# Kernel tuning notes

Measured on AMD Instinct MI355X. Metric: run time of the kernel, lower is better.

## Reference

```python
import jax, jax.numpy as jnp
import numpy as np

BATCH, NUM_MASKS, IN_DIM, OUT_DIM = 512, 16, 1024, 1024


def setup_inputs() -> dict:
    key = jax.random.key(0)
    k1, k2, k3 = jax.random.split(key, 3)
    x = jax.random.normal(k1, (BATCH, NUM_MASKS, IN_DIM), dtype=jnp.float32)
    kernel = jax.random.normal(k2, (IN_DIM, OUT_DIM), dtype=jnp.float32) * (1.0 / np.sqrt(IN_DIM))
    masks = jax.random.uniform(k3, (NUM_MASKS, IN_DIM, OUT_DIM), dtype=jnp.float32)
    return {"x": x, "kernel": kernel, "masks": masks}


def reference(x, kernel, masks):
    # masked_kernel[m, i, o] = kernel[i, o] * masks[m, i, o]
    masked_kernel = kernel[None, :, :] * masks  # (M, I, O)
    # Original tf.scan serializes batch; equivalent math is one batched einsum:
    # out[b, m, o] = sum_i x[b, m, i] * masked_kernel[m, i, o]
    # NOTE: the executed tf.scan path applies NO activation, so neither do we.
    out = jnp.einsum('bmi,mio->bmo', x, masked_kernel)  # (B, M, O)
    return out
```

## Files before the change

### kernel.cpp

```cpp
#include <hip/hip_runtime.h>
#include <hip/hip_bf16.h>


#define BATCH 512
#define NMASK 16
#define IN_D  1024
#define OUT_D 1024

using bf16x8 = __attribute__((ext_vector_type(8))) __bf16;
using bf16x4 = __attribute__((ext_vector_type(4))) __bf16;
using f32x16 = __attribute__((ext_vector_type(16))) float;
using f32x4  = __attribute__((ext_vector_type(4))) float;
using f32x2  = __attribute__((ext_vector_type(2))) float;

typedef const __attribute__((address_space(1))) void gvoid_t;
typedef __attribute__((address_space(3))) void lvoid_t;

__device__ __forceinline__ void dma16(const void* g, const void* l) {
    __builtin_amdgcn_global_load_lds((gvoid_t*)(uintptr_t)g,
                                     (lvoid_t*)(uintptr_t)l, 16, 0, 0);
}

__global__ void __launch_bounds__(256, 8)
mdl_prep_w(const float* __restrict__ Kn,
           const float* __restrict__ Mk,
           unsigned short* __restrict__ Wt)
{
    const int raw = blockIdx.x;
    const int wg  = (raw & 7) * 1024 + (raw >> 3);
    const int m  = wg >> 9;
    const int G  = (wg >> 2) & 127;
    const int cq = wg & 3;
    const int col = cq * 256 + threadIdx.x;
    const int i0  = G * 8;

    const float* mk = Mk + ((size_t)m * IN_D + i0) * OUT_D + col;
    const float* kn = Kn + (size_t)i0 * OUT_D + col;

    float a[8], b[8];
#pragma unroll
    for (int r = 0; r < 8; ++r) {
        a[r] = mk[(size_t)r * OUT_D];
        b[r] = kn[(size_t)r * OUT_D];
    }
    bf16x8 g;
#pragma unroll
    for (int r = 0; r < 8; ++r)
        g[r] = (__bf16)(a[r] * b[r]);

    *(bf16x8*)(Wt + (((size_t)m * 128 + G) * 1024 + col) * 8) = g;
}

__global__ void __launch_bounds__(512, 4)
mdl_prep_x(const float* __restrict__ X,
           unsigned short* __restrict__ Xp)
{
    const int t  = threadIdx.x;
    const int b2 = blockIdx.x;
    const int strip = b2 >> 2;
    const int Gq    = b2 & 3;
    const int m  = strip >> 3;
    const int bt = strip & 7;
    const int row = t >> 3;
    const int oc  = t & 7;

    const float* src = X + ((size_t)(bt * 64 + row) * NMASK + m) * IN_D
                         + Gq * 256 + oc * 32;
    f32x4 av[8];
#pragma unroll
    for (int q = 0; q < 8; ++q)
        av[q] = *(const f32x4*)(src + q * 4);

    unsigned short* dstS = Xp + (size_t)strip * 65536
                              + (size_t)(Gq * 32 + oc * 4) * 512 + row * 8;
#pragma unroll
    for (int j = 0; j < 4; ++j) {
        bf16x8 g;
#pragma unroll
        for (int e = 0; e < 4; ++e) {
            g[e]     = (__bf16)av[2 * j][e];
            g[4 + e] = (__bf16)av[2 * j + 1][e];
        }
        *(bf16x8*)(dstS + (size_t)j * 512) = g;
    }
}

struct Frags { bf16x8 a[2][2]; bf16x8 b[2][2]; };

__global__ void __launch_bounds__(256, 2)
mdl_gemm2(const unsigned short* __restrict__ Xp,
          const unsigned short* __restrict__ Wt,
          float* __restrict__ Out)
{
    const int t = threadIdx.x;
    const int l = t & 63;
    const int w = t >> 6;

    const int raw = blockIdx.x;
    const int wg  = (raw & 7) * 64 + (raw >> 3);
    const int v   = wg * 4 + w;
    const int m   = v >> 7;
    const int v7  = v & 127;
    const int bt  = v7 >> 4;
    const int ot  = v7 & 15;

    const unsigned short* Ap = Xp + (size_t)(m * 8 + bt) * 65536;
    const int la = (l & 31) * 8;
    const int ls = l >> 5;
    const int bcol = ot * 64 + (l & 31);

    f32x16 acc[2][2];
#pragma unroll
    for (int ti = 0; ti < 2; ++ti)
#pragma unroll
        for (int tj = 0; tj < 2; ++tj)
#pragma unroll
            for (int e = 0; e < 16; ++e)
                acc[ti][tj][e] = 0.f;

    auto LOADF = [&](Frags& F, int kb) {
#pragma unroll
        for (int s = 0; s < 2; ++s) {
            const int G = (kb >> 3) + s * 2 + ls;
            const unsigned short* ab = Ap + (size_t)G * 512 + la;
            F.a[s][0] = *(const bf16x8*)(ab);
            F.a[s][1] = *(const bf16x8*)(ab + 256);
            const unsigned short* bb =
                Wt + (((size_t)m * 128 + G) * 1024 + bcol) * 8;
            F.b[s][0] = *(const bf16x8*)(bb);
            F.b[s][1] = *(const bf16x8*)(bb + 256);
        }
    };
    auto MF = [&](Frags& F) {
#pragma unroll
        for (int s = 0; s < 2; ++s)
#pragma unroll
            for (int ti = 0; ti < 2; ++ti)
#pragma unroll
                for (int tj = 0; tj < 2; ++tj)
                    acc[ti][tj] = __builtin_amdgcn_mfma_f32_32x32x16_bf16(
                        F.a[s][ti], F.b[s][tj], acc[ti][tj], 0, 0, 0);
    };

    Frags S0, S1;
    LOADF(S0, 0);
    for (int kb = 0; kb < IN_D; kb += 64) {
        LOADF(S1, kb + 32);
        __builtin_amdgcn_sched_barrier(0);
        MF(S0);
        LOADF(S0, (kb + 64) & (IN_D - 1));
        __builtin_amdgcn_sched_barrier(0);
        MF(S1);
    }

    const int r0 = bt * 64 + 4 * ls;
    const int c0 = ot * 64 + (l & 31);
#pragma unroll
    for (int ti = 0; ti < 2; ++ti) {
#pragma unroll
        for (int tj = 0; tj < 2; ++tj) {
#pragma unroll
            for (int g = 0; g < 4; ++g) {
#pragma unroll
                for (int q = 0; q < 4; ++q) {
                    const int row = r0 + ti * 32 + g * 8 + q;
                    const int col = c0 + tj * 32;
                    Out[((size_t)row * NMASK + m) * OUT_D + col] =
                        acc[ti][tj][g * 4 + q];
                }
            }
        }
    }
}

#define FAKP 40
#define FBKP 34
#define FMFSZ (32 * 128)

__global__ void __launch_bounds__(512, 4)
mdl_fused_fallback(const float* __restrict__ X,
                   const float* __restrict__ Kn,
                   const float* __restrict__ Mk,
                   float* __restrict__ Out)
{
    __shared__ __align__(16) float          Mf[3 * FMFSZ];
    __shared__ __align__(16) unsigned short As[128 * FAKP];
    __shared__ __align__(16) unsigned short Bs[128 * FBKP];

    const int t = threadIdx.x;
    const int l = t & 63;
    const int w = t >> 6;

    const int raw = blockIdx.x;
    const int wg  = (raw & 7) * 64 + (raw >> 3);
    const int m   = wg >> 5;
    const int ob  = (wg >> 2) & 7;
    const int bb  = wg & 3;

    const int wr = w >> 2, wc = w & 3;

    f32x4 acc[4][2];
#pragma unroll
    for (int mi = 0; mi < 4; ++mi)
#pragma unroll
        for (int ni = 0; ni < 2; ++ni)
            acc[mi][ni] = (f32x4){0.f, 0.f, 0.f, 0.f};

    const int a_row = t >> 2;
    const int a_kh  = (t & 3) * 8;
    const int o2 = (t & 63) * 2;
    const int k4 = w * 4;

    const int obase = ob * 128;
    const float* Xa  = X + ((size_t)(bb * 128 + a_row) * NMASK + m) * IN_D + a_kh;
    const float* Knb = Kn + obase + o2;
    const float* Mkm = Mk + (size_t)m * IN_D * OUT_D;

    auto DMA = [&](int tile, int c) {
        const int kt = tile * 32;
#pragma unroll
        for (int j = 0; j < 2; ++j) {
            const int k = j * 16 + w * 2 + (l >> 5);
            const float* gsrc = Mkm + (size_t)(kt + k) * OUT_D + obase + (l & 31) * 4;
            dma16(gsrc, &Mf[c * FMFSZ + j * 2048 + w * 256]);
        }
    };

    DMA(0, 0);
    DMA(1, 1);
    asm volatile("s_waitcnt vmcnt(2)" ::: "memory");
    __builtin_amdgcn_sched_barrier(0);
    __builtin_amdgcn_s_barrier();
    __builtin_amdgcn_sched_barrier(0);

    int c_cur = 0, c_nxt = 1, c_far = 2;

    for (int tt = 0; tt < 32; ++tt) {
        const int kt = tt * 32;
        f32x4 xv0 = *(const f32x4*)(Xa + kt);
        f32x4 xv1 = *(const f32x4*)(Xa + kt + 4);
        f32x2 kv[4];
#pragma unroll
        for (int r = 0; r < 4; ++r)
            kv[r] = *(const f32x2*)(Knb + (size_t)(kt + k4 + r) * OUT_D);
        __builtin_amdgcn_sched_barrier(0);
        DMA((tt + 2 < 32) ? tt + 2 : 0, c_far);
        __builtin_amdgcn_sched_barrier(0);
        {
            f32x2 mvv[4];
#pragma unroll
            for (int r = 0; r < 4; ++r)
                mvv[r] = *(const f32x2*)(&Mf[c_cur * FMFSZ + (k4 + r) * 128 + o2]);
#pragma unroll
            for (int c = 0; c < 2; ++c) {
                bf16x4 vv;
#pragma unroll
                for (int r = 0; r < 4; ++r)
                    vv[r] = (__bf16)(kv[r][c] * mvv[r][c]);
                *(bf16x4*)(&Bs[(o2 + c) * FBKP + k4]) = vv;
            }
            bf16x8 va;
#pragma unroll
            for (int j = 0; j < 4; ++j) {
                va[j] = (__bf16)xv0[j]; va[4 + j] = (__bf16)xv1[j];
            }
            *(bf16x8*)(&As[a_row * FAKP + a_kh]) = va;
        }
        asm volatile("s_waitcnt lgkmcnt(0)" ::: "memory");
        __builtin_amdgcn_sched_barrier(0);
        __builtin_amdgcn_s_barrier();
        __builtin_amdgcn_sched_barrier(0);
        {
            const int kg = (l >> 4) * 8;
            bf16x8 bfv[2];
#pragma unroll
            for (int ni = 0; ni < 2; ++ni) {
                const int n = wc * 32 + ni * 16 + (l & 15);
                bf16x4 lo = *(const bf16x4*)(&Bs[n * FBKP + kg]);
                bf16x4 hi = *(const bf16x4*)(&Bs[n * FBKP + kg + 4]);
                bf16x8 f;
                f[0] = lo[0]; f[1] = lo[1]; f[2] = lo[2]; f[3] = lo[3];
                f[4] = hi[0]; f[5] = hi[1]; f[6] = hi[2]; f[7] = hi[3];
                bfv[ni] = f;
            }
#pragma unroll
            for (int mi = 0; mi < 4; ++mi) {
                const int r = wr * 64 + mi * 16 + (l & 15);
                bf16x8 af = *(const bf16x8*)(&As[r * FAKP + kg]);
#pragma unroll
                for (int ni = 0; ni < 2; ++ni)
                    acc[mi][ni] = __builtin_amdgcn_mfma_f32_16x16x32_bf16(
                        af, bfv[ni], acc[mi][ni], 0, 0, 0);
            }
        }
        asm volatile("s_waitcnt vmcnt(2)" ::: "memory");
        __builtin_amdgcn_sched_barrier(0);
        __builtin_amdgcn_s_barrier();
        __builtin_amdgcn_sched_barrier(0);
        const int tmp = c_cur; c_cur = c_nxt; c_nxt = c_far; c_far = tmp;
    }
    asm volatile("s_waitcnt vmcnt(0)" ::: "memory");

    const int r0 = bb * 128 + wr * 64 + (l >> 4) * 4;
    const int c0 = ob * 128 + wc * 32 + (l & 15);
#pragma unroll
    for (int mi = 0; mi < 4; ++mi) {
#pragma unroll
        for (int j = 0; j < 4; ++j) {
            const size_t row = (size_t)(r0 + mi * 16 + j);
            float* op = Out + (row * NMASK + m) * OUT_D + c0;
#pragma unroll
            for (int ni = 0; ni < 2; ++ni)
                op[ni * 16] = acc[mi][ni][j];
        }
    }
}

extern "C" void kernel_launch(void* const* d_in, const int* in_sizes, int n_in,
                              void* d_out, int out_size, void* d_ws, size_t ws_size,
                              hipStream_t stream) {
    (void)in_sizes; (void)n_in; (void)out_size;
    const float* X  = (const float*)d_in[0];
    const float* Kn = (const float*)d_in[1];
    const float* Mk = (const float*)d_in[2];
    float* Out = (float*)d_out;

    const size_t w_bytes = (size_t)NMASK * IN_D * OUT_D * sizeof(unsigned short);
    const size_t x_bytes = (size_t)BATCH * NMASK * IN_D * sizeof(unsigned short);

    if (ws_size >= w_bytes + x_bytes) {
        unsigned short* Wt = (unsigned short*)d_ws;
        unsigned short* Xp = (unsigned short*)d_ws + w_bytes / 2;
        mdl_prep_w<<<8192, 256, 0, stream>>>(Kn, Mk, Wt);
        mdl_prep_x<<<512, 512, 0, stream>>>(X, Xp);
        mdl_gemm2<<<512, 256, 0, stream>>>(Xp, Wt, Out);
    } else {
        mdl_fused_fallback<<<512, 512, 0, stream>>>(X, Kn, Mk, Out);
    }
}
```

Measured before the change: 61.45 us.

## Merge weight and activation prep kernels into one interleaved launch with LDS-staged X stores

Combines the two preprocessing kernels into a single launch of 4608 blocks, where every ninth block converts X and the other eight build the masked bf16 weight. This removes one kernel launch and the boundary between the two memory-bound passes, so both can stream concurrently. The X path now stages converted bf16 data through shared memory so each wave writes contiguous 1KB rows instead of scattered 16-byte chunks. It adds a barrier and LDS usage to the X blocks, and the weight blocks now use 512 threads instead of 256.

Result: faster. 54.13 us (-11.9%).

```diff
diff --git a/kernel.cpp b/kernel.cpp
--- a/kernel.cpp
+++ b/kernel.cpp
@@ -21,67 +21,80 @@
                                      (lvoid_t*)(uintptr_t)l, 16, 0, 0);
 }
 
-__global__ void __launch_bounds__(256, 8)
-mdl_prep_w(const float* __restrict__ Kn,
-           const float* __restrict__ Mk,
-           unsigned short* __restrict__ Wt)
+__global__ void __launch_bounds__(512, 4)
+mdl_prep(const float* __restrict__ X,
+         const float* __restrict__ Kn,
+         const float* __restrict__ Mk,
+         unsigned short* __restrict__ Wt,
+         unsigned short* __restrict__ Xp)
 {
+    __shared__ __align__(16) unsigned short Ls[64 * 264];
+
+    const int t   = threadIdx.x;
     const int raw = blockIdx.x;
-    const int wg  = (raw & 7) * 1024 + (raw >> 3);
-    const int m  = wg >> 9;
-    const int G  = (wg >> 2) & 127;
-    const int cq = wg & 3;
-    const int col = cq * 256 + threadIdx.x;
-    const int i0  = G * 8;
-
-    const float* mk = Mk + ((size_t)m * IN_D + i0) * OUT_D + col;
-    const float* kn = Kn + (size_t)i0 * OUT_D + col;
-
-    float a[8], b[8];
-#pragma unroll
-    for (int r = 0; r < 8; ++r) {
-        a[r] = mk[(size_t)r * OUT_D];
-        b[r] = kn[(size_t)r * OUT_D];
-    }
-    bf16x8 g;
-#pragma unroll
-    for (int r = 0; r < 8; ++r)
-        g[r] = (__bf16)(a[r] * b[r]);
-
-    *(bf16x8*)(Wt + (((size_t)m * 128 + G) * 1024 + col) * 8) = g;
-}
-
-__global__ void __launch_bounds__(512, 4)
-mdl_prep_x(const float* __restrict__ X,
-           unsigned short* __restrict__ Xp)
-{
-    const int t  = threadIdx.x;
-    const int b2 = blockIdx.x;
-    const int strip = b2 >> 2;
-    const int Gq    = b2 & 3;
-    const int m  = strip >> 3;
-    const int bt = strip & 7;
-    const int row = t >> 3;
-    const int oc  = t & 7;
-
-    const float* src = X + ((size_t)(bt * 64 + row) * NMASK + m) * IN_D
-                         + Gq * 256 + oc * 32;
-    f32x4 av[8];
-#pragma unroll
-    for (int q = 0; q < 8; ++q)
-        av[q] = *(const f32x4*)(src + q * 4);
-
-    unsigned short* dstS = Xp + (size_t)strip * 65536
-                              + (size_t)(Gq * 32 + oc * 4) * 512 + row * 8;
-#pragma unroll
-    for (int j = 0; j < 4; ++j) {
+    const int q   = raw / 9;
+    const int r9  = raw - q * 9;
+
+    if (r9 < 8) {
+        const int wg2 = q * 8 + r9;
+        const int m  = wg2 >> 8;
+        const int G  = (wg2 >> 1) & 127;
+        const int ch = wg2 & 1;
+        const int col = ch * 512 + t;
+        const int i0  = G * 8;
+
+        const float* mk = Mk + ((size_t)m * IN_D + i0) * OUT_D + col;
+        const float* kn = Kn + (size_t)i0 * OUT_D + col;
+
+        float a[8], b[8];
+#pragma unroll
+        for (int rr = 0; rr < 8; ++rr) {
+            a[rr] = mk[(size_t)rr * OUT_D];
+            b[rr] = kn[(size_t)rr * OUT_D];
+        }
         bf16x8 g;
 #pragma unroll
-        for (int e = 0; e < 4; ++e) {
-            g[e]     = (__bf16)av[2 * j][e];
-            g[4 + e] = (__bf16)av[2 * j + 1][e];
-        }
-        *(bf16x8*)(dstS + (size_t)j * 512) = g;
+        for (int rr = 0; rr < 8; ++rr)
+            g[rr] = (__bf16)(a[rr] * b[rr]);
+
+        *(bf16x8*)(Wt + (((size_t)m * 128 + G) * 1024 + col) * 8) = g;
+    } else {
+        const int strip = q >> 2;
+        const int Gq    = q & 3;
+        const int m  = strip >> 3;
+        const int bt = strip & 7;
+        const int row = t >> 3;
+        const int oc  = t & 7;
+
+        const float* src = X + ((size_t)(bt * 64 + row) * NMASK + m) * IN_D
+                             + Gq * 256 + oc * 32;
+        f32x4 av[8];
+#pragma unroll
+        for (int qq = 0; qq < 8; ++qq)
+            av[qq] = *(const f32x4*)(src + qq * 4);
+
+#pragma unroll
+        for (int j = 0; j < 4; ++j) {
+            bf16x8 g;
+#pragma unroll
+            for (int e = 0; e < 4; ++e) {
+                g[e]     = (__bf16)av[2 * j][e];
+                g[4 + e] = (__bf16)av[2 * j + 1][e];
+            }
+            *(bf16x8*)(&Ls[row * 264 + (oc * 4 + j) * 8]) = g;
+        }
+
+        __syncthreads();
+
+        const int w = t >> 6;
+        const int l = t & 63;
+        unsigned short* dstS = Xp + (size_t)strip * 65536
+                                  + (size_t)(Gq * 32 + w * 4) * 512 + l * 8;
+#pragma unroll
+        for (int u = 0; u < 4; ++u) {
+            bf16x8 g = *(const bf16x8*)(&Ls[l * 264 + (w * 4 + u) * 8]);
+            *(bf16x8*)(dstS + (size_t)u * 512) = g;
+        }
     }
 }
 
@@ -162,11 +175,11 @@
 #pragma unroll
             for (int g = 0; g < 4; ++g) {
 #pragma unroll
-                for (int q = 0; q < 4; ++q) {
-                    const int row = r0 + ti * 32 + g * 8 + q;
+                for (int qq = 0; qq < 4; ++qq) {
+                    const int row = r0 + ti * 32 + g * 8 + qq;
                     const int col = c0 + tj * 32;
                     Out[((size_t)row * NMASK + m) * OUT_D + col] =
-                        acc[ti][tj][g * 4 + q];
+                        acc[ti][tj][g * 4 + qq];
                 }
             }
         }
@@ -241,22 +254,22 @@
         f32x4 xv1 = *(const f32x4*)(Xa + kt + 4);
         f32x2 kv[4];
 #pragma unroll
-        for (int r = 0; r < 4; ++r)
-            kv[r] = *(const f32x2*)(Knb + (size_t)(kt + k4 + r) * OUT_D);
+        for (int rr = 0; rr < 4; ++rr)
+            kv[rr] = *(const f32x2*)(Knb + (size_t)(kt + k4 + rr) * OUT_D);
         __builtin_amdgcn_sched_barrier(0);
         DMA((tt + 2 < 32) ? tt + 2 : 0, c_far);
         __builtin_amdgcn_sched_barrier(0);
         {
             f32x2 mvv[4];
 #pragma unroll
-            for (int r = 0; r < 4; ++r)
-                mvv[r] = *(const f32x2*)(&Mf[c_cur * FMFSZ + (k4 + r) * 128 + o2]);
+            for (int rr = 0; rr < 4; ++rr)
+                mvv[rr] = *(const f32x2*)(&Mf[c_cur * FMFSZ + (k4 + rr) * 128 + o2]);
 #pragma unroll
             for (int c = 0; c < 2; ++c) {
                 bf16x4 vv;
 #pragma unroll
-                for (int r = 0; r < 4; ++r)
-                    vv[r] = (__bf16)(kv[r][c] * mvv[r][c]);
+                for (int rr = 0; rr < 4; ++rr)
+                    vv[rr] = (__bf16)(kv[rr][c] * mvv[rr][c]);
                 *(bf16x4*)(&Bs[(o2 + c) * FBKP + k4]) = vv;
             }
             bf16x8 va;
@@ -285,8 +298,8 @@
             }
 #pragma unroll
             for (int mi = 0; mi < 4; ++mi) {
-                const int r = wr * 64 + mi * 16 + (l & 15);
-                bf16x8 af = *(const bf16x8*)(&As[r * FAKP + kg]);
+                const int rr = wr * 64 + mi * 16 + (l & 15);
+                bf16x8 af = *(const bf16x8*)(&As[rr * FAKP + kg]);
 #pragma unroll
                 for (int ni = 0; ni < 2; ++ni)
                     acc[mi][ni] = __builtin_amdgcn_mfma_f32_16x16x32_bf16(
@@ -331,8 +344,7 @@
     if (ws_size >= w_bytes + x_bytes) {
         unsigned short* Wt = (unsigned short*)d_ws;
         unsigned short* Xp = (unsigned short*)d_ws + w_bytes / 2;
-        mdl_prep_w<<<8192, 256, 0, stream>>>(Kn, Mk, Wt);
-        mdl_prep_x<<<512, 512, 0, stream>>>(X, Xp);
+        mdl_prep<<<4608, 512, 0, stream>>>(X, Kn, Mk, Wt, Xp);
         mdl_gemm2<<<512, 256, 0, stream>>>(Xp, Wt, Out);
     } else {
         mdl_fused_fallback<<<512, 512, 0, stream>>>(X, Kn, Mk, Out);
```
